# Kernel optimization log

Measured on AMD Instinct MI355X. Metric: run time of the kernel, lower is better.

## Reference

```python
import jax, jax.numpy as jnp
import numpy as np

N = 50000   # nodes
E = 500000  # edges
S = 64      # 0e channels in node feats
V = 32      # 1o channels in node feats
R = 32      # radial/scalar edge features
MLPW = 128
AVG = 10.0  # avg_num_neighbors
SQ3 = np.float32(np.sqrt(3.0))
SQ2 = np.float32(np.sqrt(2.0))


def setup_inputs() -> dict:
    key = jax.random.key(0)
    ks = jax.random.split(key, 10)
    node_scalars = jax.random.normal(ks[0], (N, S), jnp.float32)
    node_vectors = jax.random.normal(ks[1], (N, V, 3), jnp.float32)
    ev = jax.random.normal(ks[2], (E, 3), jnp.float32)
    # l=1 spherical harmonics of unit edge vectors, component normalization (|Y1| = sqrt(3))
    edge_vec = ev / jnp.linalg.norm(ev, axis=1, keepdims=True) * SQ3
    scalar_edge_feats = jax.random.normal(ks[3], (E, R), jnp.float32)
    lengths = jax.random.uniform(ks[4], (E, 1), jnp.float32)
    senders = jax.random.randint(ks[5], (E,), 0, N, jnp.int32)
    receivers = jax.random.randint(ks[6], (E,), 0, N, jnp.int32)
    din = 2 * S + R + 1  # 161
    num_irreps = V + (S + V)  # 128 gate scalars
    def lin(k, i, o):
        return jax.random.normal(k, (i, o), jnp.float32) / np.float32(np.sqrt(i))
    return {
        "node_scalars": node_scalars, "node_vectors": node_vectors,
        "edge_vec": edge_vec, "scalar_edge_feats": scalar_edge_feats,
        "lengths": lengths, "senders": senders, "receivers": receivers,
        "W1": lin(ks[7], din, MLPW), "b1": jnp.zeros((MLPW,), jnp.float32),
        "W2": lin(ks[8], MLPW, MLPW), "b2": jnp.zeros((MLPW,), jnp.float32),
        "W3": lin(ks[9], MLPW, num_irreps), "b3": jnp.zeros((num_irreps,), jnp.float32),
    }


def reference(node_scalars, node_vectors, edge_vec, scalar_edge_feats, lengths,
              senders, receivers, W1, b1, W2, b2, W3, b3):
    # gather sender features
    s_snd = node_scalars[senders]          # [E, S]
    v_snd = node_vectors[senders]          # [E, V, 3]
    # Clebsch-Gordan tensor product with 1o edge harmonics (component normalization):
    m0 = jnp.einsum('eca,ea->ec', v_snd, edge_vec) / SQ3          # 1o x 1o -> 0e, [E, V]
    m1a = s_snd[:, :, None] * edge_vec[:, None, :]                 # 0e x 1o -> 1o, [E, S, 3]
    m1b = jnp.cross(v_snd, edge_vec[:, None, :]) / SQ2             # 1o x 1o -> 1o, [E, V, 3]
    # MLP gate on concatenated scalars
    mlp_in = jnp.concatenate([s_snd, node_scalars[receivers], scalar_edge_feats, lengths], axis=1)
    h = jax.nn.silu(mlp_in @ W1 + b1)
    h = jax.nn.silu(h @ W2 + b2)
    mix = h @ W3 + b3                                               # [E, V + S + V]
    m0 = m0 * mix[:, :V]
    m1 = jnp.concatenate([m1a, m1b], axis=1) * mix[:, V:, None]     # [E, S+V, 3]
    # scatter-add to receivers
    out0 = jax.ops.segment_sum(m0, receivers, num_segments=N)      # [N, V]
    out1 = jax.ops.segment_sum(m1, receivers, num_segments=N)      # [N, S+V, 3]
    return jnp.concatenate([out0, out1.reshape(N, -1)], axis=1) / AVG
```

## Files before the change

kernel.cpp:

```cpp
#include <hip/hip_runtime.h>

#define N_NODES 50000
#define N_EDGES 500000
#define EB 64
#define HST 136
#define W1K 176
#define OUTC 320
#define MROW 208
#define NBLK1 49
#define KP1 200
#define KH  136
#define KV  104
#define WTS 40
#define INV_SQ3 0.57735026918962576f
#define INV_SQ2 0.70710678118654752f
#define INV_AVG 0.1f

typedef short bf16x8 __attribute__((ext_vector_type(8)));
typedef unsigned short u16;
typedef u16 u16x8 __attribute__((ext_vector_type(8)));
typedef float f32x16 __attribute__((ext_vector_type(16)));

__device__ __forceinline__ unsigned cvtpk(float lo, float hi) {
    unsigned r;
    asm("v_cvt_pk_bf16_f32 %0, %1, %2" : "=v"(r) : "v"(lo), "v"(hi));
    return r;
}
__device__ __forceinline__ u16 f2bf(float f) { return (u16)cvtpk(f, f); }
__device__ __forceinline__ float bf2f(u16 h) {
    union { unsigned u; float f; } x; x.u = ((unsigned)h) << 16; return x.f;
}
__device__ __forceinline__ float fsilu(float x) {
    return x * __builtin_amdgcn_rcpf(1.f + __expf(-x));
}

__device__ __forceinline__ void stage16(const float* g, u16* l, bool v) {
    float4 a0, a1, a2, a3;
    const float4 z = make_float4(0.f, 0.f, 0.f, 0.f);
    if (v) { a0 = *(const float4*)(g);     a1 = *(const float4*)(g + 4);
             a2 = *(const float4*)(g + 8); a3 = *(const float4*)(g + 12); }
    else   { a0 = z; a1 = z; a2 = z; a3 = z; }
    uint4 p0 = { cvtpk(a0.x, a0.y), cvtpk(a0.z, a0.w), cvtpk(a1.x, a1.y), cvtpk(a1.z, a1.w) };
    uint4 p1 = { cvtpk(a2.x, a2.y), cvtpk(a2.z, a2.w), cvtpk(a3.x, a3.y), cvtpk(a3.z, a3.w) };
    *(uint4*)(l) = p0; *(uint4*)(l + 8) = p1;
}
__device__ __forceinline__ void stage8(const float* g, u16* l, bool v) {
    float4 a0, a1;
    const float4 z = make_float4(0.f, 0.f, 0.f, 0.f);
    if (v) { a0 = *(const float4*)(g); a1 = *(const float4*)(g + 4); }
    else   { a0 = z; a1 = z; }
    uint4 p0 = { cvtpk(a0.x, a0.y), cvtpk(a0.z, a0.w), cvtpk(a1.x, a1.y), cvtpk(a1.z, a1.w) };
    *(uint4*)(l) = p0;
}


__global__ void hist_kernel(const int* __restrict__ recv, int* __restrict__ counts) {
    const int e = blockIdx.x * 256 + threadIdx.x;
    if (e < N_EDGES) atomicAdd(&counts[recv[e]], 1);
}

__global__ __launch_bounds__(256) void scan_k1(const int* __restrict__ counts,
                                               int* __restrict__ rowp,
                                               int* __restrict__ partials) {
    __shared__ int sd[256];
    const int t = threadIdx.x;
    const int base = blockIdx.x * 1024 + t * 4;
    int c0 = 0, c1 = 0, c2 = 0, c3 = 0;
    if (base + 3 < N_NODES) {
        int4 v = *(const int4*)&counts[base];
        c0 = v.x; c1 = v.y; c2 = v.z; c3 = v.w;
    } else {
        if (base     < N_NODES) c0 = counts[base];
        if (base + 1 < N_NODES) c1 = counts[base + 1];
        if (base + 2 < N_NODES) c2 = counts[base + 2];
        if (base + 3 < N_NODES) c3 = counts[base + 3];
    }
    const int T = c0 + c1 + c2 + c3;
    sd[t] = T; __syncthreads();
    for (int off = 1; off < 256; off <<= 1) {
        int v = (t >= off) ? sd[t - off] : 0;
        __syncthreads();
        sd[t] += v;
        __syncthreads();
    }
    const int excl = sd[t] - T;
    if (base     < N_NODES) rowp[base]     = excl;
    if (base + 1 < N_NODES) rowp[base + 1] = excl + c0;
    if (base + 2 < N_NODES) rowp[base + 2] = excl + c0 + c1;
    if (base + 3 < N_NODES) rowp[base + 3] = excl + c0 + c1 + c2;
    if (t == 255) partials[blockIdx.x] = sd[255];
}

__global__ __launch_bounds__(64) void scan_k2(int* __restrict__ partials) {
    __shared__ int sd[64];
    const int t = threadIdx.x;
    const int v0 = (t < NBLK1) ? partials[t] : 0;
    sd[t] = v0; __syncthreads();
    for (int off = 1; off < 64; off <<= 1) {
        int v = (t >= off) ? sd[t - off] : 0;
        __syncthreads();
        sd[t] += v;
        __syncthreads();
    }
    if (t < NBLK1) partials[t] = sd[t] - v0;
}

__global__ __launch_bounds__(256) void scan_k3(int* __restrict__ rowp,
                                               const int* __restrict__ partials,
                                               int* __restrict__ cursors) {
    const int add = partials[blockIdx.x];
    const int base = blockIdx.x * 1024 + threadIdx.x * 4;
    #pragma unroll
    for (int i = 0; i < 4; ++i) {
        const int idx = base + i;
        if (idx < N_NODES) {
            const int v = rowp[idx] + add;
            rowp[idx] = v;
            cursors[idx] = v;
        }
    }
    if (blockIdx.x == 0 && threadIdx.x == 0) rowp[N_NODES] = N_EDGES;
}

__global__ void fill_kernel(const int* __restrict__ recv,
                            const int* __restrict__ snd,
                            int* __restrict__ cursors,
                            int* __restrict__ elist,
                            int* __restrict__ esnd,
                            int* __restrict__ ercv) {
    const int e = blockIdx.x * 256 + threadIdx.x;
    if (e < N_EDGES) {
        const int r = recv[e];
        const int pos = atomicAdd(&cursors[r], 1);
        elist[pos] = e;
        esnd[pos]  = snd[e];
        ercv[pos]  = r;
    }
}


#define WT_TOTAL (128 * W1K + 2 * 128 * 128)

__global__ __launch_bounds__(256)
void wcvt_kernel(const float* __restrict__ W1, const float* __restrict__ W2,
                 const float* __restrict__ W3, u16* __restrict__ wt) {
    const int i = blockIdx.x * 256 + threadIdx.x;
    if (i < 128 * W1K) {
        const int n = i / W1K, k = i - n * W1K;
        wt[i] = (k < 161) ? f2bf(W1[(size_t)k * 128 + n]) : (u16)0;
    } else if (i < 128 * W1K + 128 * 128) {
        const int j = i - 128 * W1K;
        const int n = j >> 7, k = j & 127;
        wt[i] = f2bf(W2[(size_t)k * 128 + n]);
    } else if (i < WT_TOTAL) {
        const int j = i - 128 * W1K - 128 * 128;
        const int n = j >> 7, k = j & 127;
        wt[i] = f2bf(W3[(size_t)k * 128 + n]);
    }
}


#define NS_ELEMS (N_NODES * 64)
#define NV_ELEMS (N_NODES * 96)

__global__ __launch_bounds__(256)
void nodecvt_kernel(const float* __restrict__ ns, const float* __restrict__ nv,
                    u16* __restrict__ nsb, u16* __restrict__ nvb) {
    const int i2 = (blockIdx.x * 256 + threadIdx.x) * 2;
    if (i2 < NS_ELEMS) {
        float2 v = *(const float2*)(ns + i2);
        *(unsigned*)(nsb + i2) = cvtpk(v.x, v.y);
    } else if (i2 < NS_ELEMS + NV_ELEMS) {
        const int j2 = i2 - NS_ELEMS;
        float2 v = *(const float2*)(nv + j2);
        *(unsigned*)(nvb + j2) = cvtpk(v.x, v.y);
    }
}


__global__ __launch_bounds__(256)
void edgeperm_kernel(const int* __restrict__ elist,
                     const float* __restrict__ sef,
                     const float* __restrict__ len,
                     const float* __restrict__ ev,
                     u16* __restrict__ sefp,
                     u16* __restrict__ lenp,
                     float* __restrict__ evp) {
    const int s2 = blockIdx.x * 256 + threadIdx.x;
    const int slot = s2 >> 1, h = s2 & 1;
    if (slot >= N_EDGES) return;
    const int e = elist[slot];
    const float* src = sef + (size_t)e * 32 + h * 16;
    u16* dst = sefp + (size_t)slot * 32 + h * 16;
    float4 a0 = ((const float4*)src)[0], a1 = ((const float4*)src)[1];
    float4 a2 = ((const float4*)src)[2], a3 = ((const float4*)src)[3];
    uint4 p0 = { cvtpk(a0.x, a0.y), cvtpk(a0.z, a0.w), cvtpk(a1.x, a1.y), cvtpk(a1.z, a1.w) };
    uint4 p1 = { cvtpk(a2.x, a2.y), cvtpk(a2.z, a2.w), cvtpk(a3.x, a3.y), cvtpk(a3.z, a3.w) };
    ((uint4*)dst)[0] = p0; ((uint4*)dst)[1] = p1;
    if (h == 0) {
        lenp[slot] = f2bf(len[e]);
        const float* ep = ev + (size_t)e * 3;
        float* dp = evp + (size_t)slot * 3;
        dp[0] = ep[0]; dp[1] = ep[1]; dp[2] = ep[2];
    }
}


__global__ __launch_bounds__(256, 5)
void mlp_msg_kernel(const u16* __restrict__ ns_bf,
                    const u16* __restrict__ nv_bf,
                    const int* __restrict__ esnd,
                    const int* __restrict__ ercv,
                    const u16* __restrict__ sefp,
                    const u16* __restrict__ lenp,
                    const float* __restrict__ evp,
                    const u16* __restrict__ wt,
                    const float* __restrict__ b1,
                    const float* __restrict__ b2,
                    const float* __restrict__ b3,
                    u16* __restrict__ msg, int slo, int cnt)
{
    __shared__ u16 Hb[EB * HST];

    const int t = threadIdx.x;
    const int lbase = blockIdx.x * EB;
    const int w = t >> 6, l = t & 63;
    const int lr = l & 31, lg = l >> 5;
    const int m0 = (w >> 1) * 32, n0 = (w & 1) * 64;

    const int lsA   = lbase + m0 + lr;
    const int slotA = slo + (lsA < cnt ? lsA : 0);
    const int siA = esnd[slotA];
    const int riA = ercv[slotA];

    const int me = t >> 2, q = t & 3;
    const int lsE = lbase + me;
    const bool veE = lsE < cnt;
    const int slotE = slo + (veE ? lsE : 0);
    const int siE = esnd[slotE];
    const float evx = evp[(size_t)slotE * 3 + 0];
    const float evy = evp[(size_t)slotE * 3 + 1];
    const float evz = evp[(size_t)slotE * 3 + 2];

    bf16x8 afr[11];
    {
        const u16* sp = ns_bf + (size_t)siA * 64 + lg * 8;
        const u16* rp = ns_bf + (size_t)riA * 64 + lg * 8;
        const u16* fp = sefp + (size_t)slotA * 32 + lg * 8;
        #pragma unroll
        for (int ks = 0; ks < 4; ++ks) afr[ks]     = *(const bf16x8*)(sp + ks * 16);
        #pragma unroll
        for (int ks = 0; ks < 4; ++ks) afr[4 + ks] = *(const bf16x8*)(rp + ks * 16);
        afr[8] = *(const bf16x8*)(fp);
        afr[9] = *(const bf16x8*)(fp + 16);
        bf16x8 z = (bf16x8)0;
        if (lg == 0) z[0] = (short)lenp[slotA];
        afr[10] = z;
    }

    const u16* w1t = wt;
    const u16* w2t = wt + 128 * W1K;
    const u16* w3t = w2t + 128 * 128;

    f32x16 acc0, acc1;

    #pragma unroll
    for (int i = 0; i < 16; ++i) { acc0[i] = 0.f; acc1[i] = 0.f; }
    {
        const u16* bp0 = w1t + (size_t)(n0 + lr) * W1K + lg * 8;
        const u16* bp1 = bp0 + 32 * W1K;
        #pragma unroll
        for (int ks = 0; ks < 11; ++ks) {
            bf16x8 bv0 = *(const bf16x8*)(bp0 + ks * 16);
            bf16x8 bv1 = *(const bf16x8*)(bp1 + ks * 16);
            acc0 = __builtin_amdgcn_mfma_f32_32x32x16_bf16(afr[ks], bv0, acc0, 0, 0, 0);
            acc1 = __builtin_amdgcn_mfma_f32_32x32x16_bf16(afr[ks], bv1, acc1, 0, 0, 0);
        }
    }
    {   const float bv0 = b1[n0 + lr], bv1 = b1[n0 + 32 + lr];
        #pragma unroll
        for (int r = 0; r < 16; ++r) {
            const int row = (r & 3) + 8 * (r >> 2) + 4 * lg;
            Hb[(m0 + row) * HST + n0 + lr]      = f2bf(fsilu(acc0[r] + bv0));
            Hb[(m0 + row) * HST + n0 + 32 + lr] = f2bf(fsilu(acc1[r] + bv1));
        }
    }
    __syncthreads();

    auto run_layer_lds = [&](const u16* Wg, f32x16& a0, f32x16& a1) {
        #pragma unroll
        for (int i = 0; i < 16; ++i) { a0[i] = 0.f; a1[i] = 0.f; }
        const u16* ap  = Hb + (m0 + lr) * HST + lg * 8;
        const u16* bp0 = Wg + (size_t)(n0 + lr) * 128 + lg * 8;
        const u16* bp1 = bp0 + 32 * 128;
        #pragma unroll
        for (int ks = 0; ks < 8; ++ks) {
            bf16x8 af  = *(const bf16x8*)(ap  + ks * 16);
            bf16x8 bv0 = *(const bf16x8*)(bp0 + ks * 16);
            bf16x8 bv1 = *(const bf16x8*)(bp1 + ks * 16);
            a0 = __builtin_amdgcn_mfma_f32_32x32x16_bf16(af, bv0, a0, 0, 0, 0);
            a1 = __builtin_amdgcn_mfma_f32_32x32x16_bf16(af, bv1, a1, 0, 0, 0);
        }
    };

    run_layer_lds(w2t, acc0, acc1);
    __syncthreads();
    {   const float bv0 = b2[n0 + lr], bv1 = b2[n0 + 32 + lr];
        #pragma unroll
        for (int r = 0; r < 16; ++r) {
            const int row = (r & 3) + 8 * (r >> 2) + 4 * lg;
            Hb[(m0 + row) * HST + n0 + lr]      = f2bf(fsilu(acc0[r] + bv0));
            Hb[(m0 + row) * HST + n0 + 32 + lr] = f2bf(fsilu(acc1[r] + bv1));
        }
    }
    __syncthreads();

    run_layer_lds(w3t, acc0, acc1);
    __syncthreads();
    {   const float bv0 = b3[n0 + lr], bv1 = b3[n0 + 32 + lr];
        #pragma unroll
        for (int r = 0; r < 16; ++r) {
            const int row = (r & 3) + 8 * (r >> 2) + 4 * lg;
            Hb[(m0 + row) * HST + n0 + lr]      = f2bf(acc0[r] + bv0);
            Hb[(m0 + row) * HST + n0 + 32 + lr] = f2bf(acc1[r] + bv1);
        }
    }
    __syncthreads();

    if (veE) {
        const u16* Hr = Hb + me * HST;
        u16* mrow = msg + (size_t)lsE * MROW;

        u16 sa[16], va[24];
        {
            const u16* nsrow = ns_bf + (size_t)siE * 64 + 16 * q;
            *(u16x8*)(sa)     = *(const u16x8*)(nsrow);
            *(u16x8*)(sa + 8) = *(const u16x8*)(nsrow + 8);
            const u16* nvrow = nv_bf + (size_t)siE * 96 + 24 * q;
            *(u16x8*)(va)      = *(const u16x8*)(nvrow);
            *(u16x8*)(va + 8)  = *(const u16x8*)(nvrow + 8);
            *(u16x8*)(va + 16) = *(const u16x8*)(nvrow + 16);
        }

        float m0v[8], m1bv[24];
        #pragma unroll
        for (int j = 0; j < 8; ++j) {
            const int c = 8 * q + j;
            const float vx = bf2f(va[3 * j]), vy = bf2f(va[3 * j + 1]), vz = bf2f(va[3 * j + 2]);
            m0v[j] = (vx * evx + vy * evy + vz * evz) * INV_SQ3 * bf2f(Hr[c]);
            const float gb = bf2f(Hr[96 + c]) * INV_SQ2;
            m1bv[3 * j + 0] = (vy * evz - vz * evy) * gb;
            m1bv[3 * j + 1] = (vz * evx - vx * evz) * gb;
            m1bv[3 * j + 2] = (vx * evy - vy * evx) * gb;
        }
        {   uint4 o = { cvtpk(m0v[0], m0v[1]), cvtpk(m0v[2], m0v[3]),
                        cvtpk(m0v[4], m0v[5]), cvtpk(m0v[6], m0v[7]) };
            *(uint4*)(mrow + 8 * q) = o;
        }
        {   u16* dst = mrow + 96 + 24 * q;
            uint4 o0 = { cvtpk(m1bv[0],  m1bv[1]),  cvtpk(m1bv[2],  m1bv[3]),
                         cvtpk(m1bv[4],  m1bv[5]),  cvtpk(m1bv[6],  m1bv[7])  };
            uint4 o1 = { cvtpk(m1bv[8],  m1bv[9]),  cvtpk(m1bv[10], m1bv[11]),
                         cvtpk(m1bv[12], m1bv[13]), cvtpk(m1bv[14], m1bv[15]) };
            uint4 o2 = { cvtpk(m1bv[16], m1bv[17]), cvtpk(m1bv[18], m1bv[19]),
                         cvtpk(m1bv[20], m1bv[21]), cvtpk(m1bv[22], m1bv[23]) };
            *(uint4*)(dst)      = o0;
            *(uint4*)(dst + 8)  = o1;
            *(uint4*)(dst + 16) = o2;
        }
        {   float sg[16];
            #pragma unroll
            for (int j = 0; j < 16; ++j) {
                const int k = 16 * q + j;
                sg[j] = bf2f(sa[j]) * bf2f(Hr[32 + k]);
            }
            u16* dst = mrow + 32 + 16 * q;
            uint4 o0 = { cvtpk(sg[0],  sg[1]),  cvtpk(sg[2],  sg[3]),
                         cvtpk(sg[4],  sg[5]),  cvtpk(sg[6],  sg[7])  };
            uint4 o1 = { cvtpk(sg[8],  sg[9]),  cvtpk(sg[10], sg[11]),
                         cvtpk(sg[12], sg[13]), cvtpk(sg[14], sg[15]) };
            *(uint4*)(dst)     = o0;
            *(uint4*)(dst + 8) = o1;
        }
        if (q == 0) {
            uint4 e4 = { __builtin_bit_cast(unsigned, evx),
                         __builtin_bit_cast(unsigned, evy),
                         __builtin_bit_cast(unsigned, evz), 0u };
            *(uint4*)(mrow + 192) = e4;
            uint4 z4 = { 0u, 0u, 0u, 0u };
            *(uint4*)(mrow + 200) = z4;
        }
    }
}


__global__ __launch_bounds__(256)
void msg_gather_seq(const int* __restrict__ rowp,
                    const u16* __restrict__ msg,
                    float* __restrict__ out,
                    int slo, int shi, int first)
{
    __shared__ float oacc[4][OUTC];

    const int gw = (blockIdx.x * 256 + threadIdx.x) >> 6;
    const int l  = threadIdx.x & 63;
    const bool nvalid = gw < N_NODES;

    const int rp0 = nvalid ? rowp[gw] : 0;
    const int rp1 = nvalid ? rowp[gw + 1] : 0;
    const int lo = rp0 > slo ? rp0 : slo;
    const int hi = rp1 < shi ? rp1 : shi;
    const int n  = hi > lo ? hi - lo : 0;

    const int half = (l >= 26) ? 1 : 0;
    const int sl   = l - 26 * half;
    const bool lact = (l < 52) && (sl < 24);
    const int seg  = (sl < 4) ? 0 : (sl < 12 ? 1 : 2);

    float acc[24];
    #pragma unroll
    for (int i = 0; i < 24; ++i) acc[i] = 0.f;

    const u16* mb = msg + (size_t)(lo - slo) * MROW;

    auto body = [&](int row) {
        const u16* rp = mb + (size_t)row * MROW + sl * 8;
        const u16x8 v = *(const u16x8*)rp;
        if (seg == 1) {
            const float4 e4 = *(const float4*)(mb + (size_t)row * MROW + 192);
            #pragma unroll
            for (int i = 0; i < 8; ++i) {
                const float s = bf2f(v[i]);
                acc[3 * i + 0] += s * e4.x;
                acc[3 * i + 1] += s * e4.y;
                acc[3 * i + 2] += s * e4.z;
            }
        } else {
            #pragma unroll
            for (int i = 0; i < 8; ++i) acc[i] += bf2f(v[i]);
        }
    };

    int j = 0;
    for (; j + 4 <= n; j += 4) {
        if (lact) { body(j + half); body(j + 2 + half); }
    }
    for (; j + 2 <= n; j += 2) {
        if (lact) body(j + half);
    }
    if (j < n && half == 0 && lact) body(j);

    float* oa = oacc[(threadIdx.x >> 6)];

    if (half == 0 && lact) {
        if (seg == 0) {
            #pragma unroll
            for (int i = 0; i < 8; ++i) oa[sl * 8 + i] = acc[i];
        } else if (seg == 1) {
            const int k0 = (sl - 4) * 8;
            #pragma unroll
            for (int i = 0; i < 8; ++i) {
                oa[32 + 3 * (k0 + i) + 0] = acc[3 * i + 0];
                oa[32 + 3 * (k0 + i) + 1] = acc[3 * i + 1];
                oa[32 + 3 * (k0 + i) + 2] = acc[3 * i + 2];
            }
        } else {
            const int c0 = (sl - 12) * 8;
            #pragma unroll
            for (int i = 0; i < 8; ++i) oa[224 + c0 + i] = acc[i];
        }
    }
    __syncthreads();
    if (half == 1 && lact) {
        if (seg == 0) {
            #pragma unroll
            for (int i = 0; i < 8; ++i) oa[sl * 8 + i] += acc[i];
        } else if (seg == 1) {
            const int k0 = (sl - 4) * 8;
            #pragma unroll
            for (int i = 0; i < 8; ++i) {
                oa[32 + 3 * (k0 + i) + 0] += acc[3 * i + 0];
                oa[32 + 3 * (k0 + i) + 1] += acc[3 * i + 1];
                oa[32 + 3 * (k0 + i) + 2] += acc[3 * i + 2];
            }
        } else {
            const int c0 = (sl - 12) * 8;
            #pragma unroll
            for (int i = 0; i < 8; ++i) oa[224 + c0 + i] += acc[i];
        }
    }
    __syncthreads();

    if (nvalid && l < 40) {
        float r[8];
        #pragma unroll
        for (int i = 0; i < 8; ++i) r[i] = oa[l * 8 + i] * INV_AVG;
        float* orow = out + (size_t)gw * OUTC + l * 8;
        if (first) {
            *(float4*)(orow)     = make_float4(r[0], r[1], r[2], r[3]);
            *(float4*)(orow + 4) = make_float4(r[4], r[5], r[6], r[7]);
        } else if (n > 0) {
            float4 p0 = *(const float4*)(orow);
            float4 p1 = *(const float4*)(orow + 4);
            p0.x += r[0]; p0.y += r[1]; p0.z += r[2]; p0.w += r[3];
            p1.x += r[4]; p1.y += r[5]; p1.z += r[6]; p1.w += r[7];
            *(float4*)(orow)     = p0;
            *(float4*)(orow + 4) = p1;
        }
    }
}


__global__ __launch_bounds__(256, 2)
void fused_mpconv_atomic(const float* __restrict__ node_scalars,
                         const float* __restrict__ node_vectors,
                         const float* __restrict__ edge_vec,
                         const float* __restrict__ sef,
                         const float* __restrict__ lengths,
                         const int* __restrict__ senders,
                         const int* __restrict__ receivers,
                         const float* __restrict__ W1, const float* __restrict__ b1,
                         const float* __restrict__ W2, const float* __restrict__ b2,
                         const float* __restrict__ W3, const float* __restrict__ b3,
                         float* __restrict__ out)
{
    __shared__ u16 A [EB * KP1];
    __shared__ u16 VS[EB * KV];
    __shared__ u16 Hb[EB * KH];
    __shared__ u16 Wt[2][128 * WTS];
    __shared__ float evl[3][EB];
    __shared__ int sidx[EB], ridx[EB];

    const int t = threadIdx.x;
    const int ebase = blockIdx.x * EB;

    {   const int e = t & 63, sub = t >> 6;
        const int eg = ebase + e; const bool ve = eg < N_EDGES;
        if (sub == 0)      sidx[e] = ve ? senders[eg] : 0;
        else if (sub == 1) ridx[e] = ve ? receivers[eg] : 0;
        else if (sub == 2) {
            evl[0][e] = ve ? edge_vec[(size_t)eg * 3 + 0] : 0.f;
            evl[1][e] = ve ? edge_vec[(size_t)eg * 3 + 1] : 0.f;
            evl[2][e] = ve ? edge_vec[(size_t)eg * 3 + 2] : 0.f;
        }
    }
    __syncthreads();

    {   const int me = t >> 2, q = t & 3;
        const int eg = ebase + me; const bool ve = eg < N_EDGES;
        const int si = sidx[me], ri = ridx[me];
        u16* Ar = A + me * KP1;
        stage16(node_scalars + (size_t)si * 64 + q * 16, Ar + q * 16,       ve);
        stage16(node_scalars + (size_t)ri * 64 + q * 16, Ar + 64 + q * 16,  ve);
        stage8 (sef          + (size_t)eg * 32 + q * 8,  Ar + 128 + q * 8,  ve);
        u16x8 zz = (u16x8)0;
        *(u16x8*)(Ar + 160 + q * 8) = zz;
        if (q == 0) *(u16x8*)(Ar + 192) = zz;
        stage16(node_vectors + (size_t)si * 96 + q * 24,      VS + me * KV + q * 24,      ve);
        stage8 (node_vectors + (size_t)si * 96 + q * 24 + 16, VS + me * KV + q * 24 + 16, ve);
        if (q == 0) Ar[160] = f2bf(ve ? lengths[eg] : 0.f);
    }
    __syncthreads();

    const int w  = t >> 6, l = t & 63;
    const int lr = l & 31;
    const int lg = l >> 5;
    const int m0 = (w >> 1) * 32;
    const int n0 = (w & 1) * 64;

    f32x16 acc0, acc1;
    const int n  = t & 127, ph = t >> 7;

    auto run_layer = [&](const u16* Asrc, int astr, const float* Wg, int Kr, int nsteps,
                         f32x16& a0, f32x16& a1) {
        #pragma unroll
        for (int i = 0; i < 16; ++i) { a0[i] = 0.f; a1[i] = 0.f; }
        #pragma unroll
        for (int i = 0; i < 4; ++i) {
            int kl = (i * 2 + ph) * 2;
            float v0 = (kl     < Kr) ? Wg[(size_t)kl * 128 + n]       : 0.f;
            float v1 = (kl + 1 < Kr) ? Wg[(size_t)(kl + 1) * 128 + n] : 0.f;
            *(unsigned*)&Wt[0][n * WTS + kl] = cvtpk(v0, v1);
        }
        __syncthreads();
        const u16* ap = Asrc + (m0 + lr) * astr + lg * 8;
        for (int ks = 0; ks < nsteps; ++ks) {
            const int cur = ks & 1;
            float v0[4], v1[4];
            const int kb = (ks + 1) * 16;
            if (ks + 1 < nsteps) {
                #pragma unroll
// ... 46 lines not shown
    __syncthreads();
    {   const float bv0 = b3[n0 + lr], bv1 = b3[n0 + 32 + lr];
        #pragma unroll
        for (int r = 0; r < 16; ++r) {
            const int row = (r & 3) + 8 * (r >> 2) + 4 * lg;
            Hb[(m0 + row) * KH + n0 + lr]      = f2bf(acc0[r] + bv0);
            Hb[(m0 + row) * KH + n0 + 32 + lr] = f2bf(acc1[r] + bv1);
        }
    }
    __syncthreads();

    {   const int me = t >> 2, r = t & 3;
        const int eg2 = ebase + me;
        if (eg2 < N_EDGES) {
            const int row = ridx[me];
            const float evx = evl[0][me], evy = evl[1][me], evz = evl[2][me];
            float* orow = out + (size_t)row * OUTC;
            const u16* Ar = A  + me * KP1;
            const u16* Vr = VS + me * KV;
            const u16* Hr = Hb + me * KH;
            for (int col = r; col < OUTC; col += 4) {
                float val;
                if (col < 32) {
                    const int c = col;
                    const float vx = bf2f(Vr[3 * c]), vy = bf2f(Vr[3 * c + 1]), vz = bf2f(Vr[3 * c + 2]);
                    val = (vx * evx + vy * evy + vz * evz) * INV_SQ3 * bf2f(Hr[c]);
                } else {
                    const int idx = col - 32;
                    const int k = idx / 3;
                    const int d = idx - 3 * k;
                    const float g = bf2f(Hr[32 + k]);
                    if (k < 64) {
                        const float evd = (d == 0) ? evx : ((d == 1) ? evy : evz);
                        val = bf2f(Ar[k]) * evd * g;
                    } else {
                        const int c = k - 64;
                        const float vx = bf2f(Vr[3 * c]), vy = bf2f(Vr[3 * c + 1]), vz = bf2f(Vr[3 * c + 2]);
                        float cr;
                        if (d == 0)      cr = vy * evz - vz * evy;
                        else if (d == 1) cr = vz * evx - vx * evz;
                        else             cr = vx * evy - vy * evx;
                        val = cr * INV_SQ2 * g;
                    }
                }
                atomicAdd(&orow[col], val * INV_AVG);
            }
        }
    }
}


extern "C" void kernel_launch(void* const* d_in, const int* in_sizes, int n_in,
                              void* d_out, int out_size, void* d_ws, size_t ws_size,
                              hipStream_t stream) {
    (void)in_sizes; (void)n_in;
    const float* node_scalars = (const float*)d_in[0];
    const float* node_vectors = (const float*)d_in[1];
    const float* edge_vec     = (const float*)d_in[2];
    const float* sef          = (const float*)d_in[3];
    const float* lengths      = (const float*)d_in[4];
    const int*   senders      = (const int*)d_in[5];
    const int*   receivers    = (const int*)d_in[6];
    const float* W1 = (const float*)d_in[7];
    const float* b1 = (const float*)d_in[8];
    const float* W2 = (const float*)d_in[9];
    const float* b2 = (const float*)d_in[10];
    const float* W3 = (const float*)d_in[11];
    const float* b3 = (const float*)d_in[12];
    float* out = (float*)d_out;

    auto align256 = [](size_t x) { return (x + 255) & ~(size_t)255; };

    size_t off = 0;
    const size_t o_counts  = off; off += align256((size_t)N_NODES * sizeof(int));
    const size_t o_rowp    = off; off += align256((size_t)(N_NODES + 1) * sizeof(int));
    const size_t o_cursors = off; off += align256((size_t)(N_NODES + 1) * sizeof(int));
    const size_t o_part    = off; off += align256(64 * sizeof(int));
    const size_t o_elist   = off; off += align256((size_t)N_EDGES * sizeof(int));
    const size_t o_esnd    = off; off += align256((size_t)N_EDGES * sizeof(int));
    const size_t o_ercv    = off; off += align256((size_t)N_EDGES * sizeof(int));
    const size_t o_wt      = off; off += align256((size_t)WT_TOTAL * sizeof(u16));
    const size_t o_nsb     = off; off += align256((size_t)NS_ELEMS * sizeof(u16));
    const size_t o_nvb     = off; off += align256((size_t)NV_ELEMS * sizeof(u16));
    const size_t o_sefp    = off; off += align256((size_t)N_EDGES * 32 * sizeof(u16));
    const size_t o_lenp    = off; off += align256((size_t)N_EDGES * sizeof(u16));
    const size_t o_evp     = off; off += align256((size_t)N_EDGES * 3 * sizeof(float));
    const size_t o_msg     = off;
    const size_t fixed_bytes = off;

    const size_t ROWB = (size_t)MROW * sizeof(u16);
    long Ec = 0;
    if (ws_size > fixed_bytes + (size_t)128 * ROWB) {
        size_t cap_rows = (ws_size - fixed_bytes) / ROWB;
        Ec = ((long)cap_rows - 64) / 64 * 64;
        if (Ec > N_EDGES) Ec = N_EDGES;
    }

    char* ws = (char*)d_ws;

    if (Ec >= 64) {
        int* counts  = (int*)(ws + o_counts);
        int* rowp    = (int*)(ws + o_rowp);
        int* cursors = (int*)(ws + o_cursors);
        int* part    = (int*)(ws + o_part);
        int* elist   = (int*)(ws + o_elist);
        int* esnd    = (int*)(ws + o_esnd);
        int* ercv    = (int*)(ws + o_ercv);
        u16* wt      = (u16*)(ws + o_wt);
        u16* nsb     = (u16*)(ws + o_nsb);
        u16* nvb     = (u16*)(ws + o_nvb);
        u16* sefp    = (u16*)(ws + o_sefp);
        u16* lenp    = (u16*)(ws + o_lenp);
        float* evp   = (float*)(ws + o_evp);
        u16* msg     = (u16*)(ws + o_msg);

        hipMemsetAsync(counts, 0, (size_t)N_NODES * sizeof(int), stream);
        hist_kernel<<<(N_EDGES + 255) / 256, 256, 0, stream>>>(receivers, counts);
        scan_k1<<<NBLK1, 256, 0, stream>>>(counts, rowp, part);
        scan_k2<<<1, 64, 0, stream>>>(part);
        scan_k3<<<NBLK1, 256, 0, stream>>>(rowp, part, cursors);
        fill_kernel<<<(N_EDGES + 255) / 256, 256, 0, stream>>>(
            receivers, senders, cursors, elist, esnd, ercv);
        edgeperm_kernel<<<(N_EDGES * 2 + 255) / 256, 256, 0, stream>>>(
            elist, sef, lengths, edge_vec, sefp, lenp, evp);
        wcvt_kernel<<<(WT_TOTAL + 255) / 256, 256, 0, stream>>>(W1, W2, W3, wt);
        nodecvt_kernel<<<((NS_ELEMS + NV_ELEMS) / 2 + 255) / 256, 256, 0, stream>>>(
            node_scalars, node_vectors, nsb, nvb);

        const int nchunks = (int)((N_EDGES + Ec - 1) / Ec);
        const int ggrid = (N_NODES * 64 + 255) / 256;
        for (int c = 0; c < nchunks; ++c) {
            const int slo = (int)(c * Ec);
            const int cnt = (int)((N_EDGES - slo < Ec) ? (N_EDGES - slo) : Ec);
            mlp_msg_kernel<<<(cnt + EB - 1) / EB, 256, 0, stream>>>(
                nsb, nvb, esnd, ercv, sefp, lenp, evp,
                wt, b1, b2, b3, msg, slo, cnt);
            msg_gather_seq<<<ggrid, 256, 0, stream>>>(
                rowp, msg, out, slo, slo + cnt, c == 0 ? 1 : 0);
        }
    } else {
        hipMemsetAsync(out, 0, (size_t)out_size * sizeof(float), stream);
        fused_mpconv_atomic<<<(N_EDGES + EB - 1) / EB, 256, 0, stream>>>(
            node_scalars, node_vectors, edge_vec, sef, lengths,
            senders, receivers, W1, b1, W2, b2, W3, b3, out);
    }
}
```

Baseline: 461.7 us.

## Fuse message scatter into MLP kernel with in-block segmented reduction and atomics

```diff
diff --git a/kernel.cpp b/kernel.cpp
--- a/kernel.cpp
+++ b/kernel.cpp
@@ -3,10 +3,9 @@
 #define N_NODES 50000
 #define N_EDGES 500000
 #define EB 64
-#define HST 136
+#define HST 216
 #define W1K 176
 #define OUTC 320
-#define MROW 208
 #define NBLK1 49
 #define KP1 200
 #define KH  136
@@ -162,10 +161,13 @@
 
 #define NS_ELEMS (N_NODES * 64)
 #define NV_ELEMS (N_NODES * 96)
+#define SEF_ELEMS (N_EDGES * 32)
 
 __global__ __launch_bounds__(256)
-void nodecvt_kernel(const float* __restrict__ ns, const float* __restrict__ nv,
-                    u16* __restrict__ nsb, u16* __restrict__ nvb) {
+void cvt_all_kernel(const float* __restrict__ ns, const float* __restrict__ nv,
+                    const float* __restrict__ sef,
+                    u16* __restrict__ nsb, u16* __restrict__ nvb,
+                    u16* __restrict__ sefb) {
     const int i2 = (blockIdx.x * 256 + threadIdx.x) * 2;
     if (i2 < NS_ELEMS) {
         float2 v = *(const float2*)(ns + i2);
@@ -174,53 +176,31 @@
         const int j2 = i2 - NS_ELEMS;
         float2 v = *(const float2*)(nv + j2);
         *(unsigned*)(nvb + j2) = cvtpk(v.x, v.y);
-    }
-}
-
-
-__global__ __launch_bounds__(256)
-void edgeperm_kernel(const int* __restrict__ elist,
-                     const float* __restrict__ sef,
-                     const float* __restrict__ len,
-                     const float* __restrict__ ev,
-                     u16* __restrict__ sefp,
-                     u16* __restrict__ lenp,
-                     float* __restrict__ evp) {
-    const int s2 = blockIdx.x * 256 + threadIdx.x;
-    const int slot = s2 >> 1, h = s2 & 1;
-    if (slot >= N_EDGES) return;
-    const int e = elist[slot];
-    const float* src = sef + (size_t)e * 32 + h * 16;
-    u16* dst = sefp + (size_t)slot * 32 + h * 16;
-    float4 a0 = ((const float4*)src)[0], a1 = ((const float4*)src)[1];
-    float4 a2 = ((const float4*)src)[2], a3 = ((const float4*)src)[3];
-    uint4 p0 = { cvtpk(a0.x, a0.y), cvtpk(a0.z, a0.w), cvtpk(a1.x, a1.y), cvtpk(a1.z, a1.w) };
-    uint4 p1 = { cvtpk(a2.x, a2.y), cvtpk(a2.z, a2.w), cvtpk(a3.x, a3.y), cvtpk(a3.z, a3.w) };
-    ((uint4*)dst)[0] = p0; ((uint4*)dst)[1] = p1;
-    if (h == 0) {
-        lenp[slot] = f2bf(len[e]);
-        const float* ep = ev + (size_t)e * 3;
-        float* dp = evp + (size_t)slot * 3;
-        dp[0] = ep[0]; dp[1] = ep[1]; dp[2] = ep[2];
+    } else if (i2 < NS_ELEMS + NV_ELEMS + SEF_ELEMS) {
+        const int j2 = i2 - NS_ELEMS - NV_ELEMS;
+        float2 v = *(const float2*)(sef + j2);
+        *(unsigned*)(sefb + j2) = cvtpk(v.x, v.y);
     }
 }
 
 
 __global__ __launch_bounds__(256, 5)
-void mlp_msg_kernel(const u16* __restrict__ ns_bf,
-                    const u16* __restrict__ nv_bf,
-                    const int* __restrict__ esnd,
-                    const int* __restrict__ ercv,
-                    const u16* __restrict__ sefp,
-                    const u16* __restrict__ lenp,
-                    const float* __restrict__ evp,
-                    const u16* __restrict__ wt,
-                    const float* __restrict__ b1,
-                    const float* __restrict__ b2,
-                    const float* __restrict__ b3,
-                    u16* __restrict__ msg, int slo, int cnt)
+void mlp_fused_kernel(const u16* __restrict__ ns_bf,
+                      const u16* __restrict__ nv_bf,
+                      const u16* __restrict__ sefb,
+                      const float* __restrict__ lengths,
+                      const float* __restrict__ edge_vec,
+                      const int* __restrict__ elist,
+                      const int* __restrict__ esnd,
+                      const int* __restrict__ ercv,
+                      const u16* __restrict__ wt,
+                      const float* __restrict__ b1,
+                      const float* __restrict__ b2,
+                      const float* __restrict__ b3,
+                      float* __restrict__ out, int cnt)
 {
     __shared__ u16 Hb[EB * HST];
+    __shared__ int rcv_l[EB];
 
     const int t = threadIdx.x;
     const int lbase = blockIdx.x * EB;
@@ -229,24 +209,34 @@
     const int m0 = (w >> 1) * 32, n0 = (w & 1) * 64;
 
     const int lsA   = lbase + m0 + lr;
-    const int slotA = slo + (lsA < cnt ? lsA : 0);
+    const int slotA = (lsA < cnt) ? lsA : (cnt - 1);
+    const int eidA = elist[slotA];
     const int siA = esnd[slotA];
     const int riA = ercv[slotA];
 
     const int me = t >> 2, q = t & 3;
     const int lsE = lbase + me;
     const bool veE = lsE < cnt;
-    const int slotE = slo + (veE ? lsE : 0);
+    const int slotE = veE ? lsE : (cnt - 1);
+    const int eidE = elist[slotE];
     const int siE = esnd[slotE];
-    const float evx = evp[(size_t)slotE * 3 + 0];
-    const float evy = evp[(size_t)slotE * 3 + 1];
-    const float evz = evp[(size_t)slotE * 3 + 2];
+
+    if (q == 0) {
+        rcv_l[me] = veE ? ercv[slotE] : -1;
+        const float evx = edge_vec[(size_t)eidE * 3 + 0];
+        const float evy = edge_vec[(size_t)eidE * 3 + 1];
+        const float evz = edge_vec[(size_t)eidE * 3 + 2];
+        u16* st = Hb + me * HST + 200;
+        *(float*)(st)     = evx;
+        *(float*)(st + 2) = evy;
+        *(float*)(st + 4) = evz;
+    }
 
     bf16x8 afr[11];
     {
         const u16* sp = ns_bf + (size_t)siA * 64 + lg * 8;
         const u16* rp = ns_bf + (size_t)riA * 64 + lg * 8;
-        const u16* fp = sefp + (size_t)slotA * 32 + lg * 8;
+        const u16* fp = sefb + (size_t)eidA * 32 + lg * 8;
         #pragma unroll
         for (int ks = 0; ks < 4; ++ks) afr[ks]     = *(const bf16x8*)(sp + ks * 16);
         #pragma unroll
@@ -254,7 +244,7 @@
         afr[8] = *(const bf16x8*)(fp);
         afr[9] = *(const bf16x8*)(fp + 16);
         bf16x8 z = (bf16x8)0;
-        if (lg == 0) z[0] = (short)lenp[slotA];
+        if (lg == 0) z[0] = (short)f2bf(lengths[eidA]);
         afr[10] = z;
     }
 
@@ -327,35 +317,52 @@
     }
     __syncthreads();
 
+    u16 g0[8], gs[16], gb[8], sa[16], va[24];
+    float evx, evy, evz;
+    {
+        const u16* Hr = Hb + me * HST;
+        *(u16x8*)g0       = *(const u16x8*)(Hr + 8 * q);
+        *(u16x8*)gs       = *(const u16x8*)(Hr + 32 + 16 * q);
+        *(u16x8*)(gs + 8) = *(const u16x8*)(Hr + 32 + 16 * q + 8);
+        *(u16x8*)gb       = *(const u16x8*)(Hr + 96 + 8 * q);
+        evx = *(const float*)(Hr + 200);
+        evy = *(const float*)(Hr + 202);
+        evz = *(const float*)(Hr + 204);
+        const u16* nsrow = ns_bf + (size_t)siE * 64 + 16 * q;
+        *(u16x8*)sa       = *(const u16x8*)(nsrow);
+        *(u16x8*)(sa + 8) = *(const u16x8*)(nsrow + 8);
+        const u16* nvrow = nv_bf + (size_t)siE * 96 + 24 * q;
+        *(u16x8*)va        = *(const u16x8*)(nvrow);
+        *(u16x8*)(va + 8)  = *(const u16x8*)(nvrow + 8);
+        *(u16x8*)(va + 16) = *(const u16x8*)(nvrow + 16);
+    }
+    __syncthreads();
+
     if (veE) {
-        const u16* Hr = Hb + me * HST;
-        u16* mrow = msg + (size_t)lsE * MROW;
-
-        u16 sa[16], va[24];
-        {
-            const u16* nsrow = ns_bf + (size_t)siE * 64 + 16 * q;
-            *(u16x8*)(sa)     = *(const u16x8*)(nsrow);
-            *(u16x8*)(sa + 8) = *(const u16x8*)(nsrow + 8);
-            const u16* nvrow = nv_bf + (size_t)siE * 96 + 24 * q;
-            *(u16x8*)(va)      = *(const u16x8*)(nvrow);
-            *(u16x8*)(va + 8)  = *(const u16x8*)(nvrow + 8);
-            *(u16x8*)(va + 16) = *(const u16x8*)(nvrow + 16);
-        }
-
+        u16* mrow = Hb + me * HST;
         float m0v[8], m1bv[24];
         #pragma unroll
         for (int j = 0; j < 8; ++j) {
-            const int c = 8 * q + j;
             const float vx = bf2f(va[3 * j]), vy = bf2f(va[3 * j + 1]), vz = bf2f(va[3 * j + 2]);
-            m0v[j] = (vx * evx + vy * evy + vz * evz) * INV_SQ3 * bf2f(Hr[c]);
-            const float gb = bf2f(Hr[96 + c]) * INV_SQ2;
-            m1bv[3 * j + 0] = (vy * evz - vz * evy) * gb;
-            m1bv[3 * j + 1] = (vz * evx - vx * evz) * gb;
-            m1bv[3 * j + 2] = (vx * evy - vy * evx) * gb;
+            m0v[j] = (vx * evx + vy * evy + vz * evz) * INV_SQ3 * bf2f(g0[j]);
+            const float gbv = bf2f(gb[j]) * INV_SQ2;
+            m1bv[3 * j + 0] = (vy * evz - vz * evy) * gbv;
+            m1bv[3 * j + 1] = (vz * evx - vx * evz) * gbv;
+            m1bv[3 * j + 2] = (vx * evy - vy * evx) * gbv;
         }
         {   uint4 o = { cvtpk(m0v[0], m0v[1]), cvtpk(m0v[2], m0v[3]),
                         cvtpk(m0v[4], m0v[5]), cvtpk(m0v[6], m0v[7]) };
             *(uint4*)(mrow + 8 * q) = o;
+        }
+        {   float sg[16];
+            #pragma unroll
+            for (int j = 0; j < 16; ++j) sg[j] = bf2f(sa[j]) * bf2f(gs[j]);
+            uint4 o0 = { cvtpk(sg[0],  sg[1]),  cvtpk(sg[2],  sg[3]),
+                         cvtpk(sg[4],  sg[5]),  cvtpk(sg[6],  sg[7])  };
+            uint4 o1 = { cvtpk(sg[8],  sg[9]),  cvtpk(sg[10], sg[11]),
+                         cvtpk(sg[12], sg[13]), cvtpk(sg[14], sg[15]) };
+            *(uint4*)(mrow + 32 + 16 * q)     = o0;
+            *(uint4*)(mrow + 32 + 16 * q + 8) = o1;
         }
         {   u16* dst = mrow + 96 + 24 * q;
             uint4 o0 = { cvtpk(m1bv[0],  m1bv[1]),  cvtpk(m1bv[2],  m1bv[3]),
@@ -368,145 +375,67 @@
             *(uint4*)(dst + 8)  = o1;
             *(uint4*)(dst + 16) = o2;
         }
-        {   float sg[16];
-            #pragma unroll
-            for (int j = 0; j < 16; ++j) {
-                const int k = 16 * q + j;
-                sg[j] = bf2f(sa[j]) * bf2f(Hr[32 + k]);
+    }
+    __syncthreads();
+
+    if (t < 48) {
+        const int grp = t / 24, sl = t % 24;
+        const int s0 = grp * 32;
+        float acc[24];
+        #pragma unroll
+        for (int i = 0; i < 24; ++i) acc[i] = 0.f;
+
+        auto flush = [&](int node) {
+            if (node < 0) return;
+            float* ob = out + (size_t)node * OUTC;
+            if (sl < 4) {
+                const int c0 = sl * 8;
+                #pragma unroll
+                for (int i = 0; i < 8; ++i) atomicAdd(ob + c0 + i, acc[i] * INV_AVG);
+            } else if (sl < 12) {
+                const int k0 = (sl - 4) * 8;
+                #pragma unroll
+                for (int i = 0; i < 8; ++i) {
+                    #pragma unroll
+                    for (int d = 0; d < 3; ++d)
+                        atomicAdd(ob + 32 + 3 * (k0 + i) + d, acc[3 * i + d] * INV_AVG);
+                }
+            } else {
+                const int c0 = (sl - 12) * 8;
+                #pragma unroll
+                for (int i = 0; i < 8; ++i) atomicAdd(ob + 224 + c0 + i, acc[i] * INV_AVG);
             }
-            u16* dst = mrow + 32 + 16 * q;
-            uint4 o0 = { cvtpk(sg[0],  sg[1]),  cvtpk(sg[2],  sg[3]),
-                         cvtpk(sg[4],  sg[5]),  cvtpk(sg[6],  sg[7])  };
-            uint4 o1 = { cvtpk(sg[8],  sg[9]),  cvtpk(sg[10], sg[11]),
-                         cvtpk(sg[12], sg[13]), cvtpk(sg[14], sg[15]) };
-            *(uint4*)(dst)     = o0;
-            *(uint4*)(dst + 8) = o1;
-        }
-        if (q == 0) {
-            uint4 e4 = { __builtin_bit_cast(unsigned, evx),
-                         __builtin_bit_cast(unsigned, evy),
-                         __builtin_bit_cast(unsigned, evz), 0u };
-            *(uint4*)(mrow + 192) = e4;
-            uint4 z4 = { 0u, 0u, 0u, 0u };
-            *(uint4*)(mrow + 200) = z4;
-        }
-    }
-}
-
-
-__global__ __launch_bounds__(256)
-void msg_gather_seq(const int* __restrict__ rowp,
-                    const u16* __restrict__ msg,
-                    float* __restrict__ out,
-                    int slo, int shi, int first)
-{
-    __shared__ float oacc[4][OUTC];
-
-    const int gw = (blockIdx.x * 256 + threadIdx.x) >> 6;
-    const int l  = threadIdx.x & 63;
-    const bool nvalid = gw < N_NODES;
-
-    const int rp0 = nvalid ? rowp[gw] : 0;
-    const int rp1 = nvalid ? rowp[gw + 1] : 0;
-    const int lo = rp0 > slo ? rp0 : slo;
-    const int hi = rp1 < shi ? rp1 : shi;
-    const int n  = hi > lo ? hi - lo : 0;
-
-    const int half = (l >= 26) ? 1 : 0;
-    const int sl   = l - 26 * half;
-    const bool lact = (l < 52) && (sl < 24);
-    const int seg  = (sl < 4) ? 0 : (sl < 12 ? 1 : 2);
-
-    float acc[24];
-    #pragma unroll
-    for (int i = 0; i < 24; ++i) acc[i] = 0.f;
-
-    const u16* mb = msg + (size_t)(lo - slo) * MROW;
-
-    auto body = [&](int row) {
-        const u16* rp = mb + (size_t)row * MROW + sl * 8;
-        const u16x8 v = *(const u16x8*)rp;
-        if (seg == 1) {
-            const float4 e4 = *(const float4*)(mb + (size_t)row * MROW + 192);
-            #pragma unroll
-            for (int i = 0; i < 8; ++i) {
-                const float s = bf2f(v[i]);
-                acc[3 * i + 0] += s * e4.x;
-                acc[3 * i + 1] += s * e4.y;
-                acc[3 * i + 2] += s * e4.z;
+        };
+
+        int cur = rcv_l[s0];
+        for (int s = s0; s < s0 + 32; ++s) {
+            const int nd = rcv_l[s];
+            if (nd != cur) {
+                flush(cur);
+                #pragma unroll
+                for (int i = 0; i < 24; ++i) acc[i] = 0.f;
+                cur = nd;
             }
-        } else {
-            #pragma unroll
-            for (int i = 0; i < 8; ++i) acc[i] += bf2f(v[i]);
-        }
-    };
-
-    int j = 0;
-    for (; j + 4 <= n; j += 4) {
-        if (lact) { body(j + half); body(j + 2 + half); }
-    }
-    for (; j + 2 <= n; j += 2) {
-        if (lact) body(j + half);
-    }
-    if (j < n && half == 0 && lact) body(j);
-
-    float* oa = oacc[(threadIdx.x >> 6)];
-
-    if (half == 0 && lact) {
-        if (seg == 0) {
-            #pragma unroll
-            for (int i = 0; i < 8; ++i) oa[sl * 8 + i] = acc[i];
-        } else if (seg == 1) {
-            const int k0 = (sl - 4) * 8;
-            #pragma unroll
-            for (int i = 0; i < 8; ++i) {
-                oa[32 + 3 * (k0 + i) + 0] = acc[3 * i + 0];
-                oa[32 + 3 * (k0 + i) + 1] = acc[3 * i + 1];
-                oa[32 + 3 * (k0 + i) + 2] = acc[3 * i + 2];
+            if (nd >= 0) {
+                const u16x8 v = *(const u16x8*)&Hb[s * HST + sl * 8];
+                if (sl >= 4 && sl < 12) {
+                    const float ex = *(const float*)&Hb[s * HST + 200];
+                    const float ey = *(const float*)&Hb[s * HST + 202];
+                    const float ez = *(const float*)&Hb[s * HST + 204];
+                    #pragma unroll
+                    for (int i = 0; i < 8; ++i) {
+                        const float sv = bf2f(v[i]);
+                        acc[3 * i + 0] += sv * ex;
+                        acc[3 * i + 1] += sv * ey;
+                        acc[3 * i + 2] += sv * ez;
+                    }
+                } else {
+                    #pragma unroll
+                    for (int i = 0; i < 8; ++i) acc[i] += bf2f(v[i]);
+                }
             }
-        } else {
-            const int c0 = (sl - 12) * 8;
-            #pragma unroll
-            for (int i = 0; i < 8; ++i) oa[224 + c0 + i] = acc[i];
-        }
-    }
-    __syncthreads();
-    if (half == 1 && lact) {
-        if (seg == 0) {
-            #pragma unroll
-            for (int i = 0; i < 8; ++i) oa[sl * 8 + i] += acc[i];
-        } else if (seg == 1) {
-            const int k0 = (sl - 4) * 8;
-            #pragma unroll
-            for (int i = 0; i < 8; ++i) {
-                oa[32 + 3 * (k0 + i) + 0] += acc[3 * i + 0];
-                oa[32 + 3 * (k0 + i) + 1] += acc[3 * i + 1];
-                oa[32 + 3 * (k0 + i) + 2] += acc[3 * i + 2];
-            }
-        } else {
-            const int c0 = (sl - 12) * 8;
-            #pragma unroll
-            for (int i = 0; i < 8; ++i) oa[224 + c0 + i] += acc[i];
-        }
-    }
-    __syncthreads();
-
-    if (nvalid && l < 40) {
-        float r[8];
-        #pragma unroll
-        for (int i = 0; i < 8; ++i) r[i] = oa[l * 8 + i] * INV_AVG;
-        float* orow = out + (size_t)gw * OUTC + l * 8;
-        if (first) {
-            *(float4*)(orow)     = make_float4(r[0], r[1], r[2], r[3]);
-            *(float4*)(orow + 4) = make_float4(r[4], r[5], r[6], r[7]);
-        } else if (n > 0) {
-            float4 p0 = *(const float4*)(orow);
-            float4 p1 = *(const float4*)(orow + 4);
-            p0.x += r[0]; p0.y += r[1]; p0.z += r[2]; p0.w += r[3];
-            p1.x += r[4]; p1.y += r[5]; p1.z += r[6]; p1.w += r[7];
-            *(float4*)(orow)     = p0;
-            *(float4*)(orow + 4) = p1;
-        }
+        }
+        flush(cur);
     }
 }
 
@@ -719,23 +648,12 @@
     const size_t o_wt      = off; off += align256((size_t)WT_TOTAL * sizeof(u16));
     const size_t o_nsb     = off; off += align256((size_t)NS_ELEMS * sizeof(u16));
     const size_t o_nvb     = off; off += align256((size_t)NV_ELEMS * sizeof(u16));
-    const size_t o_sefp    = off; off += align256((size_t)N_EDGES * 32 * sizeof(u16));
-    const size_t o_lenp    = off; off += align256((size_t)N_EDGES * sizeof(u16));
-    const size_t o_evp     = off; off += align256((size_t)N_EDGES * 3 * sizeof(float));
-    const size_t o_msg     = off;
-    const size_t fixed_bytes = off;
-
-    const size_t ROWB = (size_t)MROW * sizeof(u16);
-    long Ec = 0;
-    if (ws_size > fixed_bytes + (size_t)128 * ROWB) {
-        size_t cap_rows = (ws_size - fixed_bytes) / ROWB;
-        Ec = ((long)cap_rows - 64) / 64 * 64;
-        if (Ec > N_EDGES) Ec = N_EDGES;
-    }
+    const size_t o_sefb    = off; off += align256((size_t)SEF_ELEMS * sizeof(u16));
+    const size_t ws_needed = off;
 
     char* ws = (char*)d_ws;
 
-    if (Ec >= 64) {
+    if (ws_size >= ws_needed) {
         int* counts  = (int*)(ws + o_counts);
         int* rowp    = (int*)(ws + o_rowp);
         int* cursors = (int*)(ws + o_cursors);
@@ -746,35 +664,26 @@
         u16* wt      = (u16*)(ws + o_wt);
         u16* nsb     = (u16*)(ws + o_nsb);
         u16* nvb     = (u16*)(ws + o_nvb);
-        u16* sefp    = (u16*)(ws + o_sefp);
-        u16* lenp    = (u16*)(ws + o_lenp);
-        float* evp   = (float*)(ws + o_evp);
-        u16* msg     = (u16*)(ws + o_msg);
+        u16* sefb    = (u16*)(ws + o_sefb);
 
         hipMemsetAsync(counts, 0, (size_t)N_NODES * sizeof(int), stream);
+        hipMemsetAsync(out, 0, (size_t)N_NODES * OUTC * sizeof(float), stream);
         hist_kernel<<<(N_EDGES + 255) / 256, 256, 0, stream>>>(receivers, counts);
         scan_k1<<<NBLK1, 256, 0, stream>>>(counts, rowp, part);
         scan_k2<<<1, 64, 0, stream>>>(part);
         scan_k3<<<NBLK1, 256, 0, stream>>>(rowp, part, cursors);
         fill_kernel<<<(N_EDGES + 255) / 256, 256, 0, stream>>>(
             receivers, senders, cursors, elist, esnd, ercv);
-        edgeperm_kernel<<<(N_EDGES * 2 + 255) / 256, 256, 0, stream>>>(
-            elist, sef, lengths, edge_vec, sefp, lenp, evp);
         wcvt_kernel<<<(WT_TOTAL + 255) / 256, 256, 0, stream>>>(W1, W2, W3, wt);
-        nodecvt_kernel<<<((NS_ELEMS + NV_ELEMS) / 2 + 255) / 256, 256, 0, stream>>>(
-            node_scalars, node_vectors, nsb, nvb);
-
-        const int nchunks = (int)((N_EDGES + Ec - 1) / Ec);
-        const int ggrid = (N_NODES * 64 + 255) / 256;
-        for (int c = 0; c < nchunks; ++c) {
-            const int slo = (int)(c * Ec);
-            const int cnt = (int)((N_EDGES - slo < Ec) ? (N_EDGES - slo) : Ec);
-            mlp_msg_kernel<<<(cnt + EB - 1) / EB, 256, 0, stream>>>(
-                nsb, nvb, esnd, ercv, sefp, lenp, evp,
-                wt, b1, b2, b3, msg, slo, cnt);
-            msg_gather_seq<<<ggrid, 256, 0, stream>>>(
-                rowp, msg, out, slo, slo + cnt, c == 0 ? 1 : 0);
-        }
+        {
+            const int tot2 = (NS_ELEMS + NV_ELEMS + SEF_ELEMS) / 2;
+            cvt_all_kernel<<<(tot2 + 255) / 256, 256, 0, stream>>>(
+                node_scalars, node_vectors, sef, nsb, nvb, sefb);
+        }
+
+        mlp_fused_kernel<<<(N_EDGES + EB - 1) / EB, 256, 0, stream>>>(
+            nsb, nvb, sefb, lengths, edge_vec, elist, esnd, ercv,
+            wt, b1, b2, b3, out, N_EDGES);
     } else {
         hipMemsetAsync(out, 0, (size_t)out_size * sizeof(float), stream);
         fused_mpconv_atomic<<<(N_EDGES + EB - 1) / EB, 256, 0, stream>>>(
```

Result: slower. 1.129 ms (+144.4%).

## Drop edge permutation pass; gather edge features by original index in MLP kernel

Applied to the files above, without the earlier changes.

```diff
diff --git a/kernel.cpp b/kernel.cpp
--- a/kernel.cpp
+++ b/kernel.cpp
@@ -162,10 +162,13 @@
 
 #define NS_ELEMS (N_NODES * 64)
 #define NV_ELEMS (N_NODES * 96)
+#define SEF_ELEMS (N_EDGES * 32)
 
 __global__ __launch_bounds__(256)
-void nodecvt_kernel(const float* __restrict__ ns, const float* __restrict__ nv,
-                    u16* __restrict__ nsb, u16* __restrict__ nvb) {
+void cvt_all_kernel(const float* __restrict__ ns, const float* __restrict__ nv,
+                    const float* __restrict__ sef,
+                    u16* __restrict__ nsb, u16* __restrict__ nvb,
+                    u16* __restrict__ sefb) {
     const int i2 = (blockIdx.x * 256 + threadIdx.x) * 2;
     if (i2 < NS_ELEMS) {
         float2 v = *(const float2*)(ns + i2);
@@ -174,46 +177,23 @@
         const int j2 = i2 - NS_ELEMS;
         float2 v = *(const float2*)(nv + j2);
         *(unsigned*)(nvb + j2) = cvtpk(v.x, v.y);
-    }
-}
-
-
-__global__ __launch_bounds__(256)
-void edgeperm_kernel(const int* __restrict__ elist,
-                     const float* __restrict__ sef,
-                     const float* __restrict__ len,
-                     const float* __restrict__ ev,
-                     u16* __restrict__ sefp,
-                     u16* __restrict__ lenp,
-                     float* __restrict__ evp) {
-    const int s2 = blockIdx.x * 256 + threadIdx.x;
-    const int slot = s2 >> 1, h = s2 & 1;
-    if (slot >= N_EDGES) return;
-    const int e = elist[slot];
-    const float* src = sef + (size_t)e * 32 + h * 16;
-    u16* dst = sefp + (size_t)slot * 32 + h * 16;
-    float4 a0 = ((const float4*)src)[0], a1 = ((const float4*)src)[1];
-    float4 a2 = ((const float4*)src)[2], a3 = ((const float4*)src)[3];
-    uint4 p0 = { cvtpk(a0.x, a0.y), cvtpk(a0.z, a0.w), cvtpk(a1.x, a1.y), cvtpk(a1.z, a1.w) };
-    uint4 p1 = { cvtpk(a2.x, a2.y), cvtpk(a2.z, a2.w), cvtpk(a3.x, a3.y), cvtpk(a3.z, a3.w) };
-    ((uint4*)dst)[0] = p0; ((uint4*)dst)[1] = p1;
-    if (h == 0) {
-        lenp[slot] = f2bf(len[e]);
-        const float* ep = ev + (size_t)e * 3;
-        float* dp = evp + (size_t)slot * 3;
-        dp[0] = ep[0]; dp[1] = ep[1]; dp[2] = ep[2];
-    }
-}
-
-
-__global__ __launch_bounds__(256, 5)
+    } else if (i2 < NS_ELEMS + NV_ELEMS + SEF_ELEMS) {
+        const int j2 = i2 - NS_ELEMS - NV_ELEMS;
+        float2 v = *(const float2*)(sef + j2);
+        *(unsigned*)(sefb + j2) = cvtpk(v.x, v.y);
+    }
+}
+
+
+__global__ __launch_bounds__(256, 7)
 void mlp_msg_kernel(const u16* __restrict__ ns_bf,
                     const u16* __restrict__ nv_bf,
+                    const u16* __restrict__ sefb,
+                    const float* __restrict__ lengths,
+                    const float* __restrict__ edge_vec,
+                    const int* __restrict__ elist,
                     const int* __restrict__ esnd,
                     const int* __restrict__ ercv,
-                    const u16* __restrict__ sefp,
-                    const u16* __restrict__ lenp,
-                    const float* __restrict__ evp,
                     const u16* __restrict__ wt,
                     const float* __restrict__ b1,
                     const float* __restrict__ b2,
@@ -229,24 +209,23 @@
     const int m0 = (w >> 1) * 32, n0 = (w & 1) * 64;
 
     const int lsA   = lbase + m0 + lr;
-    const int slotA = slo + (lsA < cnt ? lsA : 0);
+    const int slotA = slo + ((lsA < cnt) ? lsA : (cnt - 1));
+    const int eidA = elist[slotA];
     const int siA = esnd[slotA];
     const int riA = ercv[slotA];
 
     const int me = t >> 2, q = t & 3;
     const int lsE = lbase + me;
     const bool veE = lsE < cnt;
-    const int slotE = slo + (veE ? lsE : 0);
+    const int slotE = slo + (veE ? lsE : (cnt - 1));
+    const int eidE = elist[slotE];
     const int siE = esnd[slotE];
-    const float evx = evp[(size_t)slotE * 3 + 0];
-    const float evy = evp[(size_t)slotE * 3 + 1];
-    const float evz = evp[(size_t)slotE * 3 + 2];
 
     bf16x8 afr[11];
     {
         const u16* sp = ns_bf + (size_t)siA * 64 + lg * 8;
         const u16* rp = ns_bf + (size_t)riA * 64 + lg * 8;
-        const u16* fp = sefp + (size_t)slotA * 32 + lg * 8;
+        const u16* fp = sefb + (size_t)eidA * 32 + lg * 8;
         #pragma unroll
         for (int ks = 0; ks < 4; ++ks) afr[ks]     = *(const bf16x8*)(sp + ks * 16);
         #pragma unroll
@@ -254,7 +233,7 @@
         afr[8] = *(const bf16x8*)(fp);
         afr[9] = *(const bf16x8*)(fp + 16);
         bf16x8 z = (bf16x8)0;
-        if (lg == 0) z[0] = (short)lenp[slotA];
+        if (lg == 0) z[0] = (short)f2bf(lengths[eidA]);
         afr[10] = z;
     }
 
@@ -330,6 +309,9 @@
     if (veE) {
         const u16* Hr = Hb + me * HST;
         u16* mrow = msg + (size_t)lsE * MROW;
+        const float evx = edge_vec[(size_t)eidE * 3 + 0];
+        const float evy = edge_vec[(size_t)eidE * 3 + 1];
+        const float evz = edge_vec[(size_t)eidE * 3 + 2];
 
         u16 sa[16], va[24];
         {
@@ -719,9 +701,7 @@
     const size_t o_wt      = off; off += align256((size_t)WT_TOTAL * sizeof(u16));
     const size_t o_nsb     = off; off += align256((size_t)NS_ELEMS * sizeof(u16));
     const size_t o_nvb     = off; off += align256((size_t)NV_ELEMS * sizeof(u16));
-    const size_t o_sefp    = off; off += align256((size_t)N_EDGES * 32 * sizeof(u16));
-    const size_t o_lenp    = off; off += align256((size_t)N_EDGES * sizeof(u16));
-    const size_t o_evp     = off; off += align256((size_t)N_EDGES * 3 * sizeof(float));
+    const size_t o_sefb    = off; off += align256((size_t)SEF_ELEMS * sizeof(u16));
     const size_t o_msg     = off;
     const size_t fixed_bytes = off;
 
@@ -746,9 +726,7 @@
         u16* wt      = (u16*)(ws + o_wt);
         u16* nsb     = (u16*)(ws + o_nsb);
         u16* nvb     = (u16*)(ws + o_nvb);
-        u16* sefp    = (u16*)(ws + o_sefp);
-        u16* lenp    = (u16*)(ws + o_lenp);
-        float* evp   = (float*)(ws + o_evp);
+        u16* sefb    = (u16*)(ws + o_sefb);
         u16* msg     = (u16*)(ws + o_msg);
 
         hipMemsetAsync(counts, 0, (size_t)N_NODES * sizeof(int), stream);
@@ -758,11 +736,12 @@
         scan_k3<<<NBLK1, 256, 0, stream>>>(rowp, part, cursors);
         fill_kernel<<<(N_EDGES + 255) / 256, 256, 0, stream>>>(
             receivers, senders, cursors, elist, esnd, ercv);
-        edgeperm_kernel<<<(N_EDGES * 2 + 255) / 256, 256, 0, stream>>>(
-            elist, sef, lengths, edge_vec, sefp, lenp, evp);
         wcvt_kernel<<<(WT_TOTAL + 255) / 256, 256, 0, stream>>>(W1, W2, W3, wt);
-        nodecvt_kernel<<<((NS_ELEMS + NV_ELEMS) / 2 + 255) / 256, 256, 0, stream>>>(
-            node_scalars, node_vectors, nsb, nvb);
+        {
+            const int tot2 = (NS_ELEMS + NV_ELEMS + SEF_ELEMS) / 2;
+            cvt_all_kernel<<<(tot2 + 255) / 256, 256, 0, stream>>>(
+                node_scalars, node_vectors, sef, nsb, nvb, sefb);
+        }
 
         const int nchunks = (int)((N_EDGES + Ec - 1) / Ec);
         const int ggrid = (N_NODES * 64 + 255) / 256;
@@ -770,7 +749,7 @@
             const int slo = (int)(c * Ec);
             const int cnt = (int)((N_EDGES - slo < Ec) ? (N_EDGES - slo) : Ec);
             mlp_msg_kernel<<<(cnt + EB - 1) / EB, 256, 0, stream>>>(
-                nsb, nvb, esnd, ercv, sefp, lenp, evp,
+                nsb, nvb, sefb, lengths, edge_vec, elist, esnd, ercv,
                 wt, b1, b2, b3, msg, slo, cnt);
             msg_gather_seq<<<ggrid, 256, 0, stream>>>(
                 rowp, msg, out, slo, slo + cnt, c == 0 ? 1 : 0);
```

New measurement: 471.5 us. 2.1% more time.
